# Kernel optimization log

Hardware: AMD Instinct MI355X
Metric: run time of the kernel (lower is better)

Reference implementation:

```python
import jax, jax.numpy as jnp
import numpy as np

EMBED = 128
HEADS = 32          # embed_dim // 4, forced by fuse Conv2d channel counts
HEAD_DIM = EMBED // HEADS  # 4
WS = (4, 7, 7)
N = WS[0] * WS[1] * WS[2]  # 196 tokens per window
B = 64              # batch * num_windows
SCALE = HEAD_DIM ** -0.5
EPS = 1e-5


def _rel_index():
    d, h, w = WS
    coords = np.stack(np.meshgrid(np.arange(d), np.arange(h), np.arange(w), indexing='ij'))
    flat = coords.reshape(3, -1)                       # [3, N]
    rel = (flat[:, :, None] - flat[:, None, :]).transpose(1, 2, 0).astype(np.int64)  # [N,N,3]
    rel[:, :, 0] += d - 1
    rel[:, :, 1] += h - 1
    rel[:, :, 2] += w - 1
    rel[:, :, 0] *= (2 * h - 1) * (2 * w - 1)
    rel[:, :, 1] *= (2 * w - 1)
    return rel.sum(-1).astype(np.int32)                # [N, N]


def setup_inputs() -> dict:
    key = jax.random.key(0)
    ks = jax.random.split(key, 7)
    d, h, w = WS
    tbl = (2 * d - 1) * (2 * h - 1) * (2 * w - 1)
    return {
        'x_in':      jax.random.normal(ks[0], (B, N, EMBED), dtype=jnp.float32),
        'x_in2':     jax.random.normal(ks[1], (B, N, EMBED), dtype=jnp.float32),
        'qkv_w':     jax.random.normal(ks[2], (3 * EMBED, EMBED), dtype=jnp.float32) * 0.02,
        'proj_w':    jax.random.normal(ks[3], (EMBED, EMBED), dtype=jnp.float32) * 0.02,
        'proj_b':    jnp.zeros((EMBED,), dtype=jnp.float32),
        'rpb_table': jax.random.normal(ks[4], (tbl, HEADS), dtype=jnp.float32) * 0.02,
        'fuse_w':    jax.random.normal(ks[5], (EMBED // 4, EMBED // 2), dtype=jnp.float32) * 0.1,
        'fuse_b':    jnp.zeros((EMBED // 4,), dtype=jnp.float32),
        'rel_idx':   jnp.asarray(_rel_index()),
    }


def _branch(x, qkv_w):
    b, n, c = x.shape
    qkv = (x @ qkv_w.T).reshape(b, n, 3, HEADS, c // HEADS).transpose(2, 0, 3, 1, 4)
    q, k, v = qkv[0] * SCALE, qkv[1], qkv[2]           # [b, H, n, d]
    attn = jnp.einsum('bhnd,bhmd->bhnm', q, k)         # [b, H, n, n]
    return attn, v


def reference(x_in, x_in2, qkv_w, proj_w, proj_b, rpb_table, fuse_w, fuse_b, rel_idx):
    b, n, c = x_in.shape
    attn1, v1 = _branch(x_in, qkv_w)
    attn2, v2 = _branch(x_in2, qkv_w)

    # conv-gated value fusion: Conv2d 1x1 over channel dim (= 2H) + InstanceNorm2d + ReLU + Sigmoid
    vcat = jnp.concatenate([v1, v2], axis=1)           # [b, 2H, n, d]
    v = jnp.einsum('bcnd,oc->bond', vcat, fuse_w) + fuse_b[None, :, None, None]  # [b, H, n, d]
    mu = v.mean(axis=(2, 3), keepdims=True)
    var = v.var(axis=(2, 3), keepdims=True)            # biased, as InstanceNorm2d
    v = (v - mu) * jax.lax.rsqrt(var + EPS)
    v = jax.nn.sigmoid(jax.nn.relu(v))

    # relative position bias: gather [n*n] rows of table -> [H, n, n]
    bias = rpb_table[rel_idx[:n, :n].reshape(-1)].reshape(n, n, HEADS).transpose(2, 0, 1)

    attn = jax.nn.softmax(attn1 + attn2 + bias[None], axis=-1)  # [b, H, n, n]
    x = jnp.einsum('bhnm,bhmd->bhnd', attn, v).transpose(0, 2, 1, 3).reshape(b, n, c)
    return x @ proj_w.T + proj_b
```

## Files before the change

### kernel.cpp

```cpp
#include <hip/hip_runtime.h>
#include <hip/hip_bf16.h>
#include <stdint.h>

#define NB   64
#define NTOK 196
#define NH   32
#define HD   4
#define CE   128
#define NM   38416

typedef __bf16 bf16x8 __attribute__((ext_vector_type(8)));
typedef float  f32x4  __attribute__((ext_vector_type(4)));

#define QSCALE 0.7213475204444817f
#define LOG2E  1.4426950408889634f

__device__ __forceinline__ float u2f(unsigned short u) {
    union { unsigned int i; float f; } z;
    z.i = ((unsigned int)u) << 16;
    return z.f;
}
__device__ __forceinline__ unsigned short f2u(float f) {
    union { float f; unsigned int i; } z; z.f = f;
    unsigned int x = z.i;
    return (unsigned short)((x + 0x7fffu + ((x >> 16) & 1u)) >> 16);
}

extern "C" __global__ __launch_bounds__(256) void qkv_gemm(
    const float* __restrict__ x1,
    const float* __restrict__ x2,
    const float* __restrict__ qkvw,
    unsigned short* __restrict__ Qb, unsigned short* __restrict__ Kb,
    unsigned short* __restrict__ V)
{
    __shared__ alignas(16) unsigned short AT[64][136];
    __shared__ alignas(16) unsigned short BT[64][136];
    const int tid = threadIdx.x;
    const int r0 = blockIdx.x * 64;
    const int j0 = blockIdx.y * 64;

    for (int idx = tid; idx < 2048; idx += 256) {
        int row = idx >> 5, k0 = (idx & 31) << 2;
        int r = r0 + row;
        const float* xp = (r >= 12544) ? x2 : x1;
        int rem = r - ((r >= 12544) ? 12544 : 0);
        float4 v = *(const float4*)&xp[rem * 128 + k0];
        ushort4 u; u.x = f2u(v.x); u.y = f2u(v.y); u.z = f2u(v.z); u.w = f2u(v.w);
        *(ushort4*)&AT[row][k0] = u;
    }
    for (int idx = tid; idx < 2048; idx += 256) {
        int row = idx >> 5, k0 = (idx & 31) << 2;
        float4 v = *(const float4*)&qkvw[(j0 + row) * 128 + k0];
        ushort4 u; u.x = f2u(v.x); u.y = f2u(v.y); u.z = f2u(v.z); u.w = f2u(v.w);
        *(ushort4*)&BT[row][k0] = u;
    }
    __syncthreads();

    const int lane = tid & 63, w = tid >> 6;
    const int wm = (w >> 1) * 32, wn = (w & 1) * 32;
    const int quad = lane >> 4, tcol = lane & 15;

    f32x4 acc[2][2] = {};
#pragma unroll
    for (int ks = 0; ks < 4; ++ks) {
        int k0 = ks * 32 + quad * 8;
        bf16x8 a0 = *(const bf16x8*)&AT[wm + tcol][k0];
        bf16x8 a1 = *(const bf16x8*)&AT[wm + 16 + tcol][k0];
        bf16x8 b0 = *(const bf16x8*)&BT[wn + tcol][k0];
        bf16x8 b1 = *(const bf16x8*)&BT[wn + 16 + tcol][k0];
        acc[0][0] = __builtin_amdgcn_mfma_f32_16x16x32_bf16(a0, b0, acc[0][0], 0, 0, 0);
        acc[0][1] = __builtin_amdgcn_mfma_f32_16x16x32_bf16(a0, b1, acc[0][1], 0, 0, 0);
        acc[1][0] = __builtin_amdgcn_mfma_f32_16x16x32_bf16(a1, b0, acc[1][0], 0, 0, 0);
        acc[1][1] = __builtin_amdgcn_mfma_f32_16x16x32_bf16(a1, b1, acc[1][1], 0, 0, 0);
    }

#pragma unroll
    for (int mi = 0; mi < 2; ++mi) {
#pragma unroll
        for (int ni = 0; ni < 2; ++ni) {
            int jglob = j0 + wn + ni * 16 + tcol;
            int sel = jglob >> 7;
            int jj = jglob & 127;
            int h = jj >> 2, dd = jj & 3;
#pragma unroll
            for (int reg = 0; reg < 4; ++reg) {
                int r = r0 + wm + mi * 16 + quad * 4 + reg;
                int branch = (r >= 12544) ? 1 : 0;
                int rem = r - branch * 12544;
                int b = rem / 196;
                int n = rem - b * 196;
                float v = acc[mi][ni][reg];
                if (sel == 0) {
                    Qb[((b * 32 + h) * 196 + n) * 8 + branch * 4 + dd] = f2u(v * QSCALE);
                } else if (sel == 1) {
                    Kb[((b * 32 + h) * 196 + n) * 8 + branch * 4 + dd] = f2u(v);
                } else {
                    V[(b * 64 + branch * 32 + h) * 784 + n * 4 + dd] = f2u(v);
                }
            }
        }
    }
}

extern "C" __global__ __launch_bounds__(256) void bias_build(
    const int* __restrict__ rel_idx, const float* __restrict__ rpb,
    unsigned short* __restrict__ biasM)
{
    const int qt = blockIdx.x;
    const int h  = blockIdx.y;
    const int tid = threadIdx.x, lane = tid & 63, wv = tid >> 6;
    const int quad = lane >> 4, tc = lane & 15;
    for (int nt = wv; nt < 14; nt += 4) {
        union { uint2 v; unsigned short s[4]; } e;
#pragma unroll
        for (int r = 0; r < 4; ++r) {
            int q = qt * 16 + quad * 4 + r;
            int key = nt * 16 + tc;
            unsigned short u = 0xFF80;
            if (q < 196 && key < 196) {
                int idx = rel_idx[q * 196 + key];
                u = f2u(rpb[idx * 32 + h] * LOG2E);
            }
            e.s[r] = u;
        }
        *(uint2*)(biasM + (((h * 13 + qt) * 14 + nt) * 64 + lane) * 4) = e.v;
    }
}

__device__ __forceinline__ float block_sum(float v, float* red, int tid) {
#pragma unroll
    for (int off = 32; off > 0; off >>= 1) v += __shfl_down(v, off);
    __syncthreads();
    if ((tid & 63) == 0) red[tid >> 6] = v;
    __syncthreads();
    return red[0] + red[1] + red[2] + red[3];
}

__device__ __forceinline__ float act_sig_relu(float x) {
    return x > 0.f ? __fdividef(1.f, 1.f + __expf(-x)) : 0.5f;
}

extern "C" __global__ __launch_bounds__(256) void fuse_kernel(
    const unsigned short* __restrict__ V,
    const float* __restrict__ fuse_w,
    const float* __restrict__ fuse_b,
    float* __restrict__ Vf)
{
    const int b = blockIdx.x, o0 = blockIdx.y * 2;
    const int tid = threadIdx.x;
    __shared__ float fws[2][64];
    __shared__ float red[4];
    if (tid < 128) fws[tid >> 6][tid & 63] = fuse_w[(o0 + (tid >> 6)) * 64 + (tid & 63)];
    __syncthreads();

    const unsigned short* Vb = V + b * 64 * 784;
    float a0[3] = {0.f, 0.f, 0.f}, a1[3] = {0.f, 0.f, 0.f};
    float t0 = 0.f, t1 = 0.f;
    const bool tail = tid < 16;
    for (int c = 0; c < 64; ++c) {
        float w0 = fws[0][c], w1 = fws[1][c];
        const unsigned short* Vc = Vb + c * 784;
#pragma unroll
        for (int k = 0; k < 3; ++k) {
            float x = u2f(Vc[tid + 256 * k]);
            a0[k] = fmaf(w0, x, a0[k]);
            a1[k] = fmaf(w1, x, a1[k]);
        }
        if (tail) {
            float x = u2f(Vc[tid + 768]);
            t0 = fmaf(w0, x, t0);
            t1 = fmaf(w1, x, t1);
        }
    }
    float fb0 = fuse_b[o0], fb1 = fuse_b[o0 + 1];
#pragma unroll
    for (int k = 0; k < 3; ++k) { a0[k] += fb0; a1[k] += fb1; }
    t0 += fb0; t1 += fb1;

    float s0 = a0[0] + a0[1] + a0[2] + (tail ? t0 : 0.f);
    float q0 = a0[0]*a0[0] + a0[1]*a0[1] + a0[2]*a0[2] + (tail ? t0*t0 : 0.f);
    float s1 = a1[0] + a1[1] + a1[2] + (tail ? t1 : 0.f);
    float q1 = a1[0]*a1[0] + a1[1]*a1[1] + a1[2]*a1[2] + (tail ? t1*t1 : 0.f);

    float S0 = block_sum(s0, red, tid);
    float Q0 = block_sum(q0, red, tid);
    float S1 = block_sum(s1, red, tid);
    float Q1 = block_sum(q1, red, tid);

    const float inv = 1.0f / 784.0f;
    float mu0 = S0 * inv, mu1 = S1 * inv;
    float rs0 = rsqrtf(Q0 * inv - mu0 * mu0 + 1e-5f);
    float rs1 = rsqrtf(Q1 * inv - mu1 * mu1 + 1e-5f);

    float* out0 = Vf + (b * 32 + o0) * 784;
    float* out1 = out0 + 784;
#pragma unroll
    for (int k = 0; k < 3; ++k) {
        int e = tid + 256 * k;
        out0[e] = act_sig_relu((a0[k] - mu0) * rs0);
        out1[e] = act_sig_relu((a1[k] - mu1) * rs1);
    }
    if (tail) {
        out0[tid + 768] = act_sig_relu((t0 - mu0) * rs0);
        out1[tid + 768] = act_sig_relu((t1 - mu1) * rs1);
    }
}

extern "C" __global__ __launch_bounds__(256) void attn_kernel(
    const unsigned short* __restrict__ Qb, const unsigned short* __restrict__ Kb,
    const float* __restrict__ Vf, const unsigned short* __restrict__ biasM,
    unsigned short* __restrict__ Ob)
{
    const int bh = blockIdx.x;
    const int b = bh >> 5, h = bh & 31;
    __shared__ alignas(16) unsigned short Qs[208][8];
    __shared__ alignas(16) unsigned short Ks[224][8];
    __shared__ alignas(16) unsigned short VT[16][232];
    __shared__ alignas(16) float PT[4][16][36];
    const int tid = threadIdx.x;

    const unsigned short* Qrow = Qb + bh * 196 * 8;
    const unsigned short* Krow = Kb + bh * 196 * 8;
    if (tid < 208) {
        uint4 z = {0, 0, 0, 0};
        uint4 v = (tid < 196) ? *(const uint4*)(Qrow + tid * 8) : z;
        *(uint4*)&Qs[tid][0] = v;
    }
    if (tid < 224) {
        uint4 z = {0, 0, 0, 0};
        uint4 v = (tid < 196) ? *(const uint4*)(Krow + tid * 8) : z;
        *(uint4*)&Ks[tid][0] = v;
    }
    {
        unsigned int* vtw = (unsigned int*)&VT[0][0];
        for (int i = tid; i < (16 * 232) / 2; i += 256) vtw[i] = 0u;
    }
    __syncthreads();
    if (tid < 196) {
        float4 vv = *(const float4*)(Vf + bh * 784 + tid * 4);
        VT[0][tid] = f2u(vv.x); VT[1][tid] = f2u(vv.y);
        VT[2][tid] = f2u(vv.z); VT[3][tid] = f2u(vv.w);
        VT[4][tid] = 0x3F80;
    }
    __syncthreads();

    const int lane = tid & 63, wv = tid >> 6;
    const int quad = lane >> 4, tc = lane & 15;
    float* myPT = &PT[wv][0][0];

    for (int qt = wv; qt < 13; qt += 4) {
        bf16x8 qf = *(const bf16x8*)&Qs[qt * 16 + tc][0];
        const unsigned short* bq = biasM + (unsigned)((h * 13 + qt) * 14) * 256;
        f32x4 Oacc = {};
#pragma unroll 1
        for (int kt = 0; kt < 7; ++kt) {
#pragma unroll
            for (int half = 0; half < 2; ++half) {
                int nt = kt * 2 + half;
                bf16x8 kf = {};
                if (quad == 0) kf = *(const bf16x8*)&Ks[nt * 16 + tc][0];
                uint2 bw = *(const uint2*)(bq + nt * 256 + lane * 4);
                f32x4 s;
                union { unsigned int u; float f; } c0, c1, c2, c3;
                c0.u = bw.x << 16; c1.u = bw.x & 0xffff0000u;
                c2.u = bw.y << 16; c3.u = bw.y & 0xffff0000u;
                s[0] = c0.f; s[1] = c1.f; s[2] = c2.f; s[3] = c3.f;
                s = __builtin_amdgcn_mfma_f32_16x16x32_bf16(qf, kf, s, 0, 0, 0);
                float p0 = exp2f(s[0]), p1 = exp2f(s[1]);
                float p2 = exp2f(s[2]), p3 = exp2f(s[3]);
                int col = half * 16 + tc;
                myPT[(quad * 4 + 0) * 36 + col] = p0;
                myPT[(quad * 4 + 1) * 36 + col] = p1;
                myPT[(quad * 4 + 2) * 36 + col] = p2;
                myPT[(quad * 4 + 3) * 36 + col] = p3;
            }
            float4 pa = *(const float4*)&myPT[tc * 36 + quad * 8];
            float4 pb = *(const float4*)&myPT[tc * 36 + quad * 8 + 4];
            bf16x8 pf;
            pf[0] = (__bf16)pa.x; pf[1] = (__bf16)pa.y;
            pf[2] = (__bf16)pa.z; pf[3] = (__bf16)pa.w;
            pf[4] = (__bf16)pb.x; pf[5] = (__bf16)pb.y;
            pf[6] = (__bf16)pb.z; pf[7] = (__bf16)pb.w;
            bf16x8 vfr = *(const bf16x8*)&VT[tc][kt * 32 + quad * 8];
            Oacc = __builtin_amdgcn_mfma_f32_16x16x32_bf16(pf, vfr, Oacc, 0, 0, 0);
        }
        int srcLane = quad * 16 + 4;
        float r0 = __shfl(Oacc[0], srcLane);
        float r1 = __shfl(Oacc[1], srcLane);
        float r2 = __shfl(Oacc[2], srcLane);
        float r3 = __shfl(Oacc[3], srcLane);
        if (tc < 4) {
            int qbase = qt * 16 + quad * 4;
            unsigned short* op = Ob + (b * 196 + qbase) * 128 + h * 4 + tc;
            if (qbase + 0 < 196) op[0 * 128] = f2u(Oacc[0] * __builtin_amdgcn_rcpf(r0));
            if (qbase + 1 < 196) op[1 * 128] = f2u(Oacc[1] * __builtin_amdgcn_rcpf(r1));
            if (qbase + 2 < 196) op[2 * 128] = f2u(Oacc[2] * __builtin_amdgcn_rcpf(r2));
            if (qbase + 3 < 196) op[3 * 128] = f2u(Oacc[3] * __builtin_amdgcn_rcpf(r3));
        }
    }
}

extern "C" __global__ __launch_bounds__(256) void proj_kernel(
    const unsigned short* __restrict__ Ob, const float* __restrict__ projw,
    const float* __restrict__ projb, float* __restrict__ out)
{
    __shared__ alignas(16) unsigned short AT[64][136];
    __shared__ alignas(16) unsigned short BT[64][136];
    const int tid = threadIdx.x;
    const int r0 = blockIdx.x * 64;
    const int j0 = blockIdx.y * 64;

    for (int idx = tid; idx < 1024; idx += 256) {
        int row = idx >> 4, k0 = (idx & 15) << 3;
        *(uint4*)&AT[row][k0] = *(const uint4*)&Ob[(r0 + row) * 128 + k0];
    }
    for (int idx = tid; idx < 2048; idx += 256) {
        int row = idx >> 5, k0 = (idx & 31) << 2;
        float4 v = *(const float4*)&projw[(j0 + row) * 128 + k0];
        ushort4 u; u.x = f2u(v.x); u.y = f2u(v.y); u.z = f2u(v.z); u.w = f2u(v.w);
        *(ushort4*)&BT[row][k0] = u;
    }
    __syncthreads();

    const int lane = tid & 63, w = tid >> 6;
    const int wm = (w >> 1) * 32, wn = (w & 1) * 32;
    const int quad = lane >> 4, tcol = lane & 15;

    f32x4 acc[2][2] = {};
#pragma unroll
    for (int ks = 0; ks < 4; ++ks) {
        int k0 = ks * 32 + quad * 8;
        bf16x8 a0 = *(const bf16x8*)&AT[wm + tcol][k0];
        bf16x8 a1 = *(const bf16x8*)&AT[wm + 16 + tcol][k0];
        bf16x8 b0 = *(const bf16x8*)&BT[wn + tcol][k0];
        bf16x8 b1 = *(const bf16x8*)&BT[wn + 16 + tcol][k0];
        acc[0][0] = __builtin_amdgcn_mfma_f32_16x16x32_bf16(a0, b0, acc[0][0], 0, 0, 0);
        acc[0][1] = __builtin_amdgcn_mfma_f32_16x16x32_bf16(a0, b1, acc[0][1], 0, 0, 0);
        acc[1][0] = __builtin_amdgcn_mfma_f32_16x16x32_bf16(a1, b0, acc[1][0], 0, 0, 0);
        acc[1][1] = __builtin_amdgcn_mfma_f32_16x16x32_bf16(a1, b1, acc[1][1], 0, 0, 0);
    }

#pragma unroll
    for (int mi = 0; mi < 2; ++mi) {
#pragma unroll
        for (int ni = 0; ni < 2; ++ni) {
            int j = j0 + wn + ni * 16 + tcol;
            float pb = projb[j];
#pragma unroll
            for (int reg = 0; reg < 4; ++reg) {
                int r = r0 + wm + mi * 16 + quad * 4 + reg;
                out[r * 128 + j] = acc[mi][ni][reg] + pb;
            }
        }
    }
}

extern "C" void kernel_launch(void* const* d_in, const int* in_sizes, int n_in,
                              void* d_out, int out_size, void* d_ws, size_t ws_size,
                              hipStream_t stream)
{
    const float* x1    = (const float*)d_in[0];
    const float* x2    = (const float*)d_in[1];
    const float* qkvw  = (const float*)d_in[2];
    const float* projw = (const float*)d_in[3];
    const float* projb = (const float*)d_in[4];
    const float* rpb   = (const float*)d_in[5];
    const float* fw    = (const float*)d_in[6];
    const float* fb    = (const float*)d_in[7];
    const int*   rel   = (const int*)d_in[8];
    float* out = (float*)d_out;

    char* w = (char*)d_ws;
    unsigned short* Qb  = (unsigned short*)(w);
    unsigned short* Kb  = (unsigned short*)(w + 6422528);
    unsigned short* V   = (unsigned short*)(w + 12845056);
    float*          Vf  = (float*)(w + 19267584);
    unsigned short* bM  = (unsigned short*)(w + 25690112);
    unsigned short* Ob  = (unsigned short*)(w + 28672000);

    qkv_gemm  <<<dim3(392, 6), dim3(256), 0, stream>>>(x1, x2, qkvw, Qb, Kb, V);
    bias_build<<<dim3(13, 32), dim3(256), 0, stream>>>(rel, rpb, bM);
    fuse_kernel<<<dim3(64, 16), dim3(256), 0, stream>>>(V, fw, fb, Vf);
    attn_kernel<<<dim3(2048),   dim3(256), 0, stream>>>(Qb, Kb, Vf, bM, Ob);
    proj_kernel<<<dim3(196, 2), dim3(256), 0, stream>>>(Ob, projw, projb, out);
}
```

Before: 189.2 us.

## Transpose MFMA operands to vectorize QKV stores and keep attention probabilities in registers

The QKV GEMM now swaps its MFMA operands so each lane holds four consecutive head-dim outputs, which lets it write packed 8-byte stores instead of scattered 2-byte stores. The bias layout is transposed to match a transposed score computation (K as A operand, Q as B operand). The attention kernel drops the shared-memory P staging buffer and instead shuffles bf16-packed exponentials across lanes with ds_bpermute, then feeds them straight into the PV MFMA. V fragments are preloaded into registers and the inner loop is fully unrolled. This removes LDS round-trips and narrow global stores, at the cost of more register pressure and more cross-lane permute work.

```diff
diff --git a/kernel.cpp b/kernel.cpp
--- a/kernel.cpp
+++ b/kernel.cpp
@@ -51,6 +51,291 @@
     for (int idx = tid; idx < 2048; idx += 256) {
         int row = idx >> 5, k0 = (idx & 31) << 2;
         float4 v = *(const float4*)&qkvw[(j0 + row) * 128 + k0];
+        ushort4 u; u.x = f2u(v.x); u.y = f2u(v.y); u.z = f2u(v.z); u.w = f2u(v.w);
+        *(ushort4*)&BT[row][k0] = u;
+    }
+    __syncthreads();
+
+    const int lane = tid & 63, w = tid >> 6;
+    const int wj = (w >> 1) * 32;
+    const int wt = (w & 1) * 32;
+    const int quad = lane >> 4, tc = lane & 15;
+
+    f32x4 acc[2][2] = {};
+#pragma unroll
+    for (int ks = 0; ks < 4; ++ks) {
+        int k0 = ks * 32 + quad * 8;
+        bf16x8 a0 = *(const bf16x8*)&BT[wj + tc][k0];
+        bf16x8 a1 = *(const bf16x8*)&BT[wj + 16 + tc][k0];
+        bf16x8 b0 = *(const bf16x8*)&AT[wt + tc][k0];
+        bf16x8 b1 = *(const bf16x8*)&AT[wt + 16 + tc][k0];
+        acc[0][0] = __builtin_amdgcn_mfma_f32_16x16x32_bf16(a0, b0, acc[0][0], 0, 0, 0);
+        acc[0][1] = __builtin_amdgcn_mfma_f32_16x16x32_bf16(a0, b1, acc[0][1], 0, 0, 0);
+        acc[1][0] = __builtin_amdgcn_mfma_f32_16x16x32_bf16(a1, b0, acc[1][0], 0, 0, 0);
+        acc[1][1] = __builtin_amdgcn_mfma_f32_16x16x32_bf16(a1, b1, acc[1][1], 0, 0, 0);
+    }
+
+    const int sel = j0 >> 7;
+#pragma unroll
+    for (int mi = 0; mi < 2; ++mi) {
+        int jbase = (j0 + wj + mi * 16 + quad * 4) & 127;
+        int hh = jbase >> 2;
+#pragma unroll
+        for (int ni = 0; ni < 2; ++ni) {
+            int tok = r0 + wt + ni * 16 + tc;
+            int branch = (tok >= 12544) ? 1 : 0;
+            int rem = tok - branch * 12544;
+            int bb = rem / 196;
+            int nn = rem - bb * 196;
+            union { uint2 v; unsigned short s[4]; } pk2;
+            if (sel == 0) {
+#pragma unroll
+                for (int r = 0; r < 4; ++r) pk2.s[r] = f2u(acc[mi][ni][r] * QSCALE);
+                *(uint2*)&Qb[((bb * 32 + hh) * 196 + nn) * 8 + branch * 4] = pk2.v;
+            } else if (sel == 1) {
+#pragma unroll
+                for (int r = 0; r < 4; ++r) pk2.s[r] = f2u(acc[mi][ni][r]);
+                *(uint2*)&Kb[((bb * 32 + hh) * 196 + nn) * 8 + branch * 4] = pk2.v;
+            } else {
+#pragma unroll
+                for (int r = 0; r < 4; ++r) pk2.s[r] = f2u(acc[mi][ni][r]);
+                *(uint2*)&V[(bb * 64 + branch * 32 + hh) * 784 + nn * 4] = pk2.v;
+            }
+        }
+    }
+}
+
+extern "C" __global__ __launch_bounds__(256) void bias_build(
+    const int* __restrict__ rel_idx, const float* __restrict__ rpb,
+    unsigned short* __restrict__ biasM)
+{
+    const int qt = blockIdx.x;
+    const int h  = blockIdx.y;
+    const int tid = threadIdx.x, lane = tid & 63, wv = tid >> 6;
+    const int quad = lane >> 4, tc = lane & 15;
+    for (int nt = wv; nt < 14; nt += 4) {
+        union { uint2 v; unsigned short s[4]; } e;
+#pragma unroll
+        for (int r = 0; r < 4; ++r) {
+            int q   = qt * 16 + tc;
+            int key = nt * 16 + quad * 4 + r;
+            unsigned short u = 0xFF80;
+            if (q < 196 && key < 196) {
+                int idx = rel_idx[q * 196 + key];
+                u = f2u(rpb[idx * 32 + h] * LOG2E);
+            }
+            e.s[r] = u;
+        }
+        *(uint2*)(biasM + (((h * 13 + qt) * 14 + nt) * 64 + lane) * 4) = e.v;
+    }
+}
+
+__device__ __forceinline__ float block_sum(float v, float* red, int tid) {
+#pragma unroll
+    for (int off = 32; off > 0; off >>= 1) v += __shfl_down(v, off);
+    __syncthreads();
+    if ((tid & 63) == 0) red[tid >> 6] = v;
+    __syncthreads();
+    return red[0] + red[1] + red[2] + red[3];
+}
+
+__device__ __forceinline__ float act_sig_relu(float x) {
+    return x > 0.f ? __fdividef(1.f, 1.f + __expf(-x)) : 0.5f;
+}
+
+extern "C" __global__ __launch_bounds__(256) void fuse_kernel(
+    const unsigned short* __restrict__ V,
+    const float* __restrict__ fuse_w,
+    const float* __restrict__ fuse_b,
+    float* __restrict__ Vf)
+{
+    const int b = blockIdx.x, o0 = blockIdx.y * 2;
+    const int tid = threadIdx.x;
+    __shared__ float fws[2][64];
+    __shared__ float red[4];
+    if (tid < 128) fws[tid >> 6][tid & 63] = fuse_w[(o0 + (tid >> 6)) * 64 + (tid & 63)];
+    __syncthreads();
+
+    const unsigned short* Vb = V + b * 64 * 784;
+    float a0[3] = {0.f, 0.f, 0.f}, a1[3] = {0.f, 0.f, 0.f};
+    float t0 = 0.f, t1 = 0.f;
+    const bool tail = tid < 16;
+    for (int c = 0; c < 64; ++c) {
+        float w0 = fws[0][c], w1 = fws[1][c];
+        const unsigned short* Vc = Vb + c * 784;
+#pragma unroll
+        for (int k = 0; k < 3; ++k) {
+            float x = u2f(Vc[tid + 256 * k]);
+            a0[k] = fmaf(w0, x, a0[k]);
+            a1[k] = fmaf(w1, x, a1[k]);
+        }
+        if (tail) {
+            float x = u2f(Vc[tid + 768]);
+            t0 = fmaf(w0, x, t0);
+            t1 = fmaf(w1, x, t1);
+        }
+    }
+    float fb0 = fuse_b[o0], fb1 = fuse_b[o0 + 1];
+#pragma unroll
+    for (int k = 0; k < 3; ++k) { a0[k] += fb0; a1[k] += fb1; }
+    t0 += fb0; t1 += fb1;
+
+    float s0 = a0[0] + a0[1] + a0[2] + (tail ? t0 : 0.f);
+    float q0 = a0[0]*a0[0] + a0[1]*a0[1] + a0[2]*a0[2] + (tail ? t0*t0 : 0.f);
+    float s1 = a1[0] + a1[1] + a1[2] + (tail ? t1 : 0.f);
+    float q1 = a1[0]*a1[0] + a1[1]*a1[1] + a1[2]*a1[2] + (tail ? t1*t1 : 0.f);
+
+    float S0 = block_sum(s0, red, tid);
+    float Q0 = block_sum(q0, red, tid);
+    float S1 = block_sum(s1, red, tid);
+    float Q1 = block_sum(q1, red, tid);
+
+    const float inv = 1.0f / 784.0f;
+    float mu0 = S0 * inv, mu1 = S1 * inv;
+    float rs0 = rsqrtf(Q0 * inv - mu0 * mu0 + 1e-5f);
+    float rs1 = rsqrtf(Q1 * inv - mu1 * mu1 + 1e-5f);
+
+    float* out0 = Vf + (b * 32 + o0) * 784;
+    float* out1 = out0 + 784;
+#pragma unroll
+    for (int k = 0; k < 3; ++k) {
+        int e = tid + 256 * k;
+        out0[e] = act_sig_relu((a0[k] - mu0) * rs0);
+        out1[e] = act_sig_relu((a1[k] - mu1) * rs1);
+    }
+    if (tail) {
+        out0[tid + 768] = act_sig_relu((t0 - mu0) * rs0);
+        out1[tid + 768] = act_sig_relu((t1 - mu1) * rs1);
+    }
+}
+
+extern "C" __global__ __launch_bounds__(256) void attn_kernel(
+    const unsigned short* __restrict__ Qb, const unsigned short* __restrict__ Kb,
+    const float* __restrict__ Vf, const unsigned short* __restrict__ biasM,
+    unsigned short* __restrict__ Ob)
+{
+    const int bh = blockIdx.x;
+    const int b = bh >> 5, h = bh & 31;
+    __shared__ alignas(16) unsigned short Qs[208][8];
+    __shared__ alignas(16) unsigned short Ks[224][8];
+    __shared__ alignas(16) unsigned short VT[16][232];
+    const int tid = threadIdx.x;
+
+    const unsigned short* Qrow = Qb + bh * 196 * 8;
+    const unsigned short* Krow = Kb + bh * 196 * 8;
+    if (tid < 208) {
+        uint4 z = {0, 0, 0, 0};
+        uint4 v = (tid < 196) ? *(const uint4*)(Qrow + tid * 8) : z;
+        *(uint4*)&Qs[tid][0] = v;
+    }
+    if (tid < 224) {
+        uint4 z = {0, 0, 0, 0};
+        uint4 v = (tid < 196) ? *(const uint4*)(Krow + tid * 8) : z;
+        *(uint4*)&Ks[tid][0] = v;
+    }
+    {
+        unsigned int* vtw = (unsigned int*)&VT[0][0];
+        for (int i = tid; i < (16 * 232) / 2; i += 256) vtw[i] = 0u;
+    }
+    __syncthreads();
+    if (tid < 196) {
+        float4 vv = *(const float4*)(Vf + bh * 784 + tid * 4);
+        VT[0][tid] = f2u(vv.x); VT[1][tid] = f2u(vv.y);
+        VT[2][tid] = f2u(vv.z); VT[3][tid] = f2u(vv.w);
+        VT[4][tid] = 0x3F80;
+    }
+    __syncthreads();
+
+    const int lane = tid & 63, wv = tid >> 6;
+    const int quad = lane >> 4, tc = lane & 15;
+
+    bf16x8 vfr[7];
+#pragma unroll
+    for (int kt = 0; kt < 7; ++kt)
+        vfr[kt] = *(const bf16x8*)&VT[tc][kt * 32 + quad * 8];
+
+    const int srcA = ((quad & 1) * 32 + tc) * 4;
+    const int srcB = srcA + 64;
+    const bool useT1 = quad >= 2;
+
+    const unsigned short* bias_hq0 = biasM + (h * 13) * 3584;
+
+    for (int qt = wv; qt < 13; qt += 4) {
+        bf16x8 bq = {};
+        if (quad == 0) bq = *(const bf16x8*)&Qs[qt * 16 + tc][0];
+        const unsigned short* bq_bias = bias_hq0 + qt * 3584;
+        f32x4 Oacc = {};
+#pragma unroll
+        for (int kt = 0; kt < 7; ++kt) {
+            uint2 bw0 = *(const uint2*)(bq_bias + (kt * 2 + 0) * 256 + lane * 4);
+            uint2 bw1 = *(const uint2*)(bq_bias + (kt * 2 + 1) * 256 + lane * 4);
+            f32x4 s0, s1;
+            {
+                union { unsigned int u; float f; } c;
+                c.u = bw0.x << 16;        s0[0] = c.f;
+                c.u = bw0.x & 0xffff0000u; s0[1] = c.f;
+                c.u = bw0.y << 16;        s0[2] = c.f;
+                c.u = bw0.y & 0xffff0000u; s0[3] = c.f;
+                c.u = bw1.x << 16;        s1[0] = c.f;
+                c.u = bw1.x & 0xffff0000u; s1[1] = c.f;
+                c.u = bw1.y << 16;        s1[2] = c.f;
+                c.u = bw1.y & 0xffff0000u; s1[3] = c.f;
+            }
+            bf16x8 a0 = *(const bf16x8*)&Ks[(kt * 2 + 0) * 16 + tc][0];
+            bf16x8 a1 = *(const bf16x8*)&Ks[(kt * 2 + 1) * 16 + tc][0];
+            s0 = __builtin_amdgcn_mfma_f32_16x16x32_bf16(a0, bq, s0, 0, 0, 0);
+            s1 = __builtin_amdgcn_mfma_f32_16x16x32_bf16(a1, bq, s1, 0, 0, 0);
+            union { unsigned int u; __bf16 hh[2]; } t0d0, t0d1, t1d0, t1d1;
+            t0d0.hh[0] = (__bf16)exp2f(s0[0]); t0d0.hh[1] = (__bf16)exp2f(s0[1]);
+            t0d1.hh[0] = (__bf16)exp2f(s0[2]); t0d1.hh[1] = (__bf16)exp2f(s0[3]);
+            t1d0.hh[0] = (__bf16)exp2f(s1[0]); t1d0.hh[1] = (__bf16)exp2f(s1[1]);
+            t1d1.hh[0] = (__bf16)exp2f(s1[2]); t1d1.hh[1] = (__bf16)exp2f(s1[3]);
+            int p0a = __builtin_amdgcn_ds_bpermute(srcA, (int)t0d0.u);
+            int p0b = __builtin_amdgcn_ds_bpermute(srcA, (int)t1d0.u);
+            int p1a = __builtin_amdgcn_ds_bpermute(srcA, (int)t0d1.u);
+            int p1b = __builtin_amdgcn_ds_bpermute(srcA, (int)t1d1.u);
+            int p2a = __builtin_amdgcn_ds_bpermute(srcB, (int)t0d0.u);
+            int p2b = __builtin_amdgcn_ds_bpermute(srcB, (int)t1d0.u);
+            int p3a = __builtin_amdgcn_ds_bpermute(srcB, (int)t0d1.u);
+            int p3b = __builtin_amdgcn_ds_bpermute(srcB, (int)t1d1.u);
+            union { int d[4]; bf16x8 v; } pf;
+            pf.d[0] = useT1 ? p0b : p0a;
+            pf.d[1] = useT1 ? p1b : p1a;
+            pf.d[2] = useT1 ? p2b : p2a;
+            pf.d[3] = useT1 ? p3b : p3a;
+            Oacc = __builtin_amdgcn_mfma_f32_16x16x32_bf16(vfr[kt], pf.v, Oacc, 0, 0, 0);
+        }
+        float rs = __shfl(Oacc[0], 16 + tc);
+        int q = qt * 16 + tc;
+        if (quad == 0 && q < 196) {
+            float inv = __builtin_amdgcn_rcpf(rs);
+            union { uint2 v; unsigned short s[4]; } pk2;
+            pk2.s[0] = f2u(Oacc[0] * inv);
+            pk2.s[1] = f2u(Oacc[1] * inv);
+            pk2.s[2] = f2u(Oacc[2] * inv);
+            pk2.s[3] = f2u(Oacc[3] * inv);
+            *(uint2*)&Ob[(b * 196 + q) * 128 + h * 4] = pk2.v;
+        }
+    }
+}
+
+extern "C" __global__ __launch_bounds__(256) void proj_kernel(
+    const unsigned short* __restrict__ Ob, const float* __restrict__ projw,
+    const float* __restrict__ projb, float* __restrict__ out)
+{
+    __shared__ alignas(16) unsigned short AT[64][136];
+    __shared__ alignas(16) unsigned short BT[64][136];
+    const int tid = threadIdx.x;
+    const int r0 = blockIdx.x * 64;
+    const int j0 = blockIdx.y * 64;
+
+    for (int idx = tid; idx < 1024; idx += 256) {
+        int row = idx >> 4, k0 = (idx & 15) << 3;
+        *(uint4*)&AT[row][k0] = *(const uint4*)&Ob[(r0 + row) * 128 + k0];
+    }
+    for (int idx = tid; idx < 2048; idx += 256) {
+        int row = idx >> 5, k0 = (idx & 31) << 2;
+        float4 v = *(const float4*)&projw[(j0 + row) * 128 + k0];
         ushort4 u; u.x = f2u(v.x); u.y = f2u(v.y); u.z = f2u(v.z); u.w = f2u(v.w);
         *(ushort4*)&BT[row][k0] = u;
     }
@@ -78,272 +363,6 @@
     for (int mi = 0; mi < 2; ++mi) {
 #pragma unroll
         for (int ni = 0; ni < 2; ++ni) {
-            int jglob = j0 + wn + ni * 16 + tcol;
-            int sel = jglob >> 7;
-            int jj = jglob & 127;
-            int h = jj >> 2, dd = jj & 3;
-#pragma unroll
-            for (int reg = 0; reg < 4; ++reg) {
-                int r = r0 + wm + mi * 16 + quad * 4 + reg;
-                int branch = (r >= 12544) ? 1 : 0;
-                int rem = r - branch * 12544;
-                int b = rem / 196;
-                int n = rem - b * 196;
-                float v = acc[mi][ni][reg];
-                if (sel == 0) {
-                    Qb[((b * 32 + h) * 196 + n) * 8 + branch * 4 + dd] = f2u(v * QSCALE);
-                } else if (sel == 1) {
-                    Kb[((b * 32 + h) * 196 + n) * 8 + branch * 4 + dd] = f2u(v);
-                } else {
-                    V[(b * 64 + branch * 32 + h) * 784 + n * 4 + dd] = f2u(v);
-                }
-            }
-        }
-    }
-}
-
-extern "C" __global__ __launch_bounds__(256) void bias_build(
-    const int* __restrict__ rel_idx, const float* __restrict__ rpb,
-    unsigned short* __restrict__ biasM)
-{
-    const int qt = blockIdx.x;
-    const int h  = blockIdx.y;
-    const int tid = threadIdx.x, lane = tid & 63, wv = tid >> 6;
-    const int quad = lane >> 4, tc = lane & 15;
-    for (int nt = wv; nt < 14; nt += 4) {
-        union { uint2 v; unsigned short s[4]; } e;
-#pragma unroll
-        for (int r = 0; r < 4; ++r) {
-            int q = qt * 16 + quad * 4 + r;
-            int key = nt * 16 + tc;
-            unsigned short u = 0xFF80;
-            if (q < 196 && key < 196) {
-                int idx = rel_idx[q * 196 + key];
-                u = f2u(rpb[idx * 32 + h] * LOG2E);
-            }
-            e.s[r] = u;
-        }
-        *(uint2*)(biasM + (((h * 13 + qt) * 14 + nt) * 64 + lane) * 4) = e.v;
-    }
-}
-
-__device__ __forceinline__ float block_sum(float v, float* red, int tid) {
-#pragma unroll
-    for (int off = 32; off > 0; off >>= 1) v += __shfl_down(v, off);
-    __syncthreads();
-    if ((tid & 63) == 0) red[tid >> 6] = v;
-    __syncthreads();
-    return red[0] + red[1] + red[2] + red[3];
-}
-
-__device__ __forceinline__ float act_sig_relu(float x) {
-    return x > 0.f ? __fdividef(1.f, 1.f + __expf(-x)) : 0.5f;
-}
-
-extern "C" __global__ __launch_bounds__(256) void fuse_kernel(
-    const unsigned short* __restrict__ V,
-    const float* __restrict__ fuse_w,
-    const float* __restrict__ fuse_b,
-    float* __restrict__ Vf)
-{
-    const int b = blockIdx.x, o0 = blockIdx.y * 2;
-    const int tid = threadIdx.x;
-    __shared__ float fws[2][64];
-    __shared__ float red[4];
-    if (tid < 128) fws[tid >> 6][tid & 63] = fuse_w[(o0 + (tid >> 6)) * 64 + (tid & 63)];
-    __syncthreads();
-
-    const unsigned short* Vb = V + b * 64 * 784;
-    float a0[3] = {0.f, 0.f, 0.f}, a1[3] = {0.f, 0.f, 0.f};
-    float t0 = 0.f, t1 = 0.f;
-    const bool tail = tid < 16;
-    for (int c = 0; c < 64; ++c) {
-        float w0 = fws[0][c], w1 = fws[1][c];
-        const unsigned short* Vc = Vb + c * 784;
-#pragma unroll
-        for (int k = 0; k < 3; ++k) {
-            float x = u2f(Vc[tid + 256 * k]);
-            a0[k] = fmaf(w0, x, a0[k]);
-            a1[k] = fmaf(w1, x, a1[k]);
-        }
-        if (tail) {
-            float x = u2f(Vc[tid + 768]);
-            t0 = fmaf(w0, x, t0);
-            t1 = fmaf(w1, x, t1);
-        }
-    }
-    float fb0 = fuse_b[o0], fb1 = fuse_b[o0 + 1];
-#pragma unroll
-    for (int k = 0; k < 3; ++k) { a0[k] += fb0; a1[k] += fb1; }
-    t0 += fb0; t1 += fb1;
-
-    float s0 = a0[0] + a0[1] + a0[2] + (tail ? t0 : 0.f);
-    float q0 = a0[0]*a0[0] + a0[1]*a0[1] + a0[2]*a0[2] + (tail ? t0*t0 : 0.f);
-    float s1 = a1[0] + a1[1] + a1[2] + (tail ? t1 : 0.f);
-    float q1 = a1[0]*a1[0] + a1[1]*a1[1] + a1[2]*a1[2] + (tail ? t1*t1 : 0.f);
-
-    float S0 = block_sum(s0, red, tid);
-    float Q0 = block_sum(q0, red, tid);
-    float S1 = block_sum(s1, red, tid);
-    float Q1 = block_sum(q1, red, tid);
-
-    const float inv = 1.0f / 784.0f;
-    float mu0 = S0 * inv, mu1 = S1 * inv;
-    float rs0 = rsqrtf(Q0 * inv - mu0 * mu0 + 1e-5f);
-    float rs1 = rsqrtf(Q1 * inv - mu1 * mu1 + 1e-5f);
-
-    float* out0 = Vf + (b * 32 + o0) * 784;
-    float* out1 = out0 + 784;
-#pragma unroll
-    for (int k = 0; k < 3; ++k) {
-        int e = tid + 256 * k;
-        out0[e] = act_sig_relu((a0[k] - mu0) * rs0);
-        out1[e] = act_sig_relu((a1[k] - mu1) * rs1);
-    }
-    if (tail) {
-        out0[tid + 768] = act_sig_relu((t0 - mu0) * rs0);
-        out1[tid + 768] = act_sig_relu((t1 - mu1) * rs1);
-    }
-}
-
-extern "C" __global__ __launch_bounds__(256) void attn_kernel(
-    const unsigned short* __restrict__ Qb, const unsigned short* __restrict__ Kb,
-    const float* __restrict__ Vf, const unsigned short* __restrict__ biasM,
-    unsigned short* __restrict__ Ob)
-{
-    const int bh = blockIdx.x;
-    const int b = bh >> 5, h = bh & 31;
-    __shared__ alignas(16) unsigned short Qs[208][8];
-    __shared__ alignas(16) unsigned short Ks[224][8];
-    __shared__ alignas(16) unsigned short VT[16][232];
-    __shared__ alignas(16) float PT[4][16][36];
-    const int tid = threadIdx.x;
-
-    const unsigned short* Qrow = Qb + bh * 196 * 8;
-    const unsigned short* Krow = Kb + bh * 196 * 8;
-    if (tid < 208) {
-        uint4 z = {0, 0, 0, 0};
-        uint4 v = (tid < 196) ? *(const uint4*)(Qrow + tid * 8) : z;
-        *(uint4*)&Qs[tid][0] = v;
-    }
-    if (tid < 224) {
-        uint4 z = {0, 0, 0, 0};
-        uint4 v = (tid < 196) ? *(const uint4*)(Krow + tid * 8) : z;
-        *(uint4*)&Ks[tid][0] = v;
-    }
-    {
-        unsigned int* vtw = (unsigned int*)&VT[0][0];
-        for (int i = tid; i < (16 * 232) / 2; i += 256) vtw[i] = 0u;
-    }
-    __syncthreads();
-    if (tid < 196) {
-        float4 vv = *(const float4*)(Vf + bh * 784 + tid * 4);
-        VT[0][tid] = f2u(vv.x); VT[1][tid] = f2u(vv.y);
-        VT[2][tid] = f2u(vv.z); VT[3][tid] = f2u(vv.w);
-        VT[4][tid] = 0x3F80;
-    }
-    __syncthreads();
-
-    const int lane = tid & 63, wv = tid >> 6;
-    const int quad = lane >> 4, tc = lane & 15;
-    float* myPT = &PT[wv][0][0];
-
-    for (int qt = wv; qt < 13; qt += 4) {
-        bf16x8 qf = *(const bf16x8*)&Qs[qt * 16 + tc][0];
-        const unsigned short* bq = biasM + (unsigned)((h * 13 + qt) * 14) * 256;
-        f32x4 Oacc = {};
-#pragma unroll 1
-        for (int kt = 0; kt < 7; ++kt) {
-#pragma unroll
-            for (int half = 0; half < 2; ++half) {
-                int nt = kt * 2 + half;
-                bf16x8 kf = {};
-                if (quad == 0) kf = *(const bf16x8*)&Ks[nt * 16 + tc][0];
-                uint2 bw = *(const uint2*)(bq + nt * 256 + lane * 4);
-                f32x4 s;
-                union { unsigned int u; float f; } c0, c1, c2, c3;
-                c0.u = bw.x << 16; c1.u = bw.x & 0xffff0000u;
-                c2.u = bw.y << 16; c3.u = bw.y & 0xffff0000u;
-                s[0] = c0.f; s[1] = c1.f; s[2] = c2.f; s[3] = c3.f;
-                s = __builtin_amdgcn_mfma_f32_16x16x32_bf16(qf, kf, s, 0, 0, 0);
-                float p0 = exp2f(s[0]), p1 = exp2f(s[1]);
-                float p2 = exp2f(s[2]), p3 = exp2f(s[3]);
-                int col = half * 16 + tc;
-                myPT[(quad * 4 + 0) * 36 + col] = p0;
-                myPT[(quad * 4 + 1) * 36 + col] = p1;
-                myPT[(quad * 4 + 2) * 36 + col] = p2;
-                myPT[(quad * 4 + 3) * 36 + col] = p3;
-            }
-            float4 pa = *(const float4*)&myPT[tc * 36 + quad * 8];
-            float4 pb = *(const float4*)&myPT[tc * 36 + quad * 8 + 4];
-            bf16x8 pf;
-            pf[0] = (__bf16)pa.x; pf[1] = (__bf16)pa.y;
-            pf[2] = (__bf16)pa.z; pf[3] = (__bf16)pa.w;
-            pf[4] = (__bf16)pb.x; pf[5] = (__bf16)pb.y;
-            pf[6] = (__bf16)pb.z; pf[7] = (__bf16)pb.w;
-            bf16x8 vfr = *(const bf16x8*)&VT[tc][kt * 32 + quad * 8];
-            Oacc = __builtin_amdgcn_mfma_f32_16x16x32_bf16(pf, vfr, Oacc, 0, 0, 0);
-        }
-        int srcLane = quad * 16 + 4;
-        float r0 = __shfl(Oacc[0], srcLane);
-        float r1 = __shfl(Oacc[1], srcLane);
-        float r2 = __shfl(Oacc[2], srcLane);
-        float r3 = __shfl(Oacc[3], srcLane);
-        if (tc < 4) {
-            int qbase = qt * 16 + quad * 4;
-            unsigned short* op = Ob + (b * 196 + qbase) * 128 + h * 4 + tc;
-            if (qbase + 0 < 196) op[0 * 128] = f2u(Oacc[0] * __builtin_amdgcn_rcpf(r0));
-            if (qbase + 1 < 196) op[1 * 128] = f2u(Oacc[1] * __builtin_amdgcn_rcpf(r1));
-            if (qbase + 2 < 196) op[2 * 128] = f2u(Oacc[2] * __builtin_amdgcn_rcpf(r2));
-            if (qbase + 3 < 196) op[3 * 128] = f2u(Oacc[3] * __builtin_amdgcn_rcpf(r3));
-        }
-    }
-}
-
-extern "C" __global__ __launch_bounds__(256) void proj_kernel(
-    const unsigned short* __restrict__ Ob, const float* __restrict__ projw,
-    const float* __restrict__ projb, float* __restrict__ out)
-{
-    __shared__ alignas(16) unsigned short AT[64][136];
-    __shared__ alignas(16) unsigned short BT[64][136];
-    const int tid = threadIdx.x;
-    const int r0 = blockIdx.x * 64;
-    const int j0 = blockIdx.y * 64;
-
-    for (int idx = tid; idx < 1024; idx += 256) {
-        int row = idx >> 4, k0 = (idx & 15) << 3;
-        *(uint4*)&AT[row][k0] = *(const uint4*)&Ob[(r0 + row) * 128 + k0];
-    }
-    for (int idx = tid; idx < 2048; idx += 256) {
-        int row = idx >> 5, k0 = (idx & 31) << 2;
-        float4 v = *(const float4*)&projw[(j0 + row) * 128 + k0];
-        ushort4 u; u.x = f2u(v.x); u.y = f2u(v.y); u.z = f2u(v.z); u.w = f2u(v.w);
-        *(ushort4*)&BT[row][k0] = u;
-    }
-    __syncthreads();
-
-    const int lane = tid & 63, w = tid >> 6;
-    const int wm = (w >> 1) * 32, wn = (w & 1) * 32;
-    const int quad = lane >> 4, tcol = lane & 15;
-
-    f32x4 acc[2][2] = {};
-#pragma unroll
-    for (int ks = 0; ks < 4; ++ks) {
-        int k0 = ks * 32 + quad * 8;
-        bf16x8 a0 = *(const bf16x8*)&AT[wm + tcol][k0];
-        bf16x8 a1 = *(const bf16x8*)&AT[wm + 16 + tcol][k0];
-        bf16x8 b0 = *(const bf16x8*)&BT[wn + tcol][k0];
-        bf16x8 b1 = *(const bf16x8*)&BT[wn + 16 + tcol][k0];
-        acc[0][0] = __builtin_amdgcn_mfma_f32_16x16x32_bf16(a0, b0, acc[0][0], 0, 0, 0);
-        acc[0][1] = __builtin_amdgcn_mfma_f32_16x16x32_bf16(a0, b1, acc[0][1], 0, 0, 0);
-        acc[1][0] = __builtin_amdgcn_mfma_f32_16x16x32_bf16(a1, b0, acc[1][0], 0, 0, 0);
-        acc[1][1] = __builtin_amdgcn_mfma_f32_16x16x32_bf16(a1, b1, acc[1][1], 0, 0, 0);
-    }
-
-#pragma unroll
-    for (int mi = 0; mi < 2; ++mi) {
-#pragma unroll
-        for (int ni = 0; ni < 2; ++ni) {
             int j = j0 + wn + ni * 16 + tcol;
             float pb = projb[j];
 #pragma unroll
```

Result: faster. 174.0 us (-8.0%).
